# Kernel optimization log

Measured on AMD Instinct MI355X. Metric: run time of the kernel, lower is better.

The kernel has to match this reference:

```python
import jax, jax.numpy as jnp
import numpy as np

N_EMBD = 768
N_HEAD = 12
B, T = 4, 2048
EPS = 1e-5


def layernorm(x, w, b):
    mu = jnp.mean(x, axis=-1, keepdims=True)
    var = jnp.mean(jnp.square(x - mu), axis=-1, keepdims=True)
    return (x - mu) * jax.lax.rsqrt(var + EPS) * w + b


def setup_inputs() -> dict:
    key = jax.random.key(0)
    ks = jax.random.split(key, 6)
    C = N_EMBD
    s = 0.02
    return {
        "x": jax.random.normal(ks[0], (B, T, C), jnp.float32),
        "ln1_w": jnp.ones((C,), jnp.float32),
        "ln1_b": jnp.zeros((C,), jnp.float32),
        "W_qkv": jax.random.normal(ks[1], (C, 3 * C), jnp.float32) * s,
        "b_qkv": jnp.zeros((3 * C,), jnp.float32),
        "W_attnproj": jax.random.normal(ks[2], (C, C), jnp.float32) * s,
        "b_attnproj": jnp.zeros((C,), jnp.float32),
        "ln2_w": jnp.ones((C,), jnp.float32),
        "ln2_b": jnp.zeros((C,), jnp.float32),
        "W_fc": jax.random.normal(ks[3], (C, 4 * C), jnp.float32) * s,
        "b_fc": jnp.zeros((4 * C,), jnp.float32),
        "W_mlpproj": jax.random.normal(ks[4], (4 * C, C), jnp.float32) * s,
        "b_mlpproj": jnp.zeros((C,), jnp.float32),
    }


def reference(x, ln1_w, ln1_b, W_qkv, b_qkv, W_attnproj, b_attnproj,
              ln2_w, ln2_b, W_fc, b_fc, W_mlpproj, b_mlpproj):
    Bx, Tx, C = x.shape
    H = N_HEAD
    Dh = C // H

    # --- attention branch ---
    h = layernorm(x, ln1_w, ln1_b)
    qkv = h @ W_qkv + b_qkv                       # [B, T, 3C]
    q, k, v = jnp.split(qkv, 3, axis=-1)
    q = q.reshape(Bx, Tx, H, Dh).transpose(0, 2, 1, 3)  # [B, H, T, Dh]
    k = k.reshape(Bx, Tx, H, Dh).transpose(0, 2, 1, 3)
    v = v.reshape(Bx, Tx, H, Dh).transpose(0, 2, 1, 3)
    att = jnp.einsum('bhqd,bhkd->bhqk', q, k) * (1.0 / np.sqrt(Dh))
    att = jax.nn.softmax(att, axis=-1)            # full softmax attention (no mask)
    y = jnp.einsum('bhqk,bhkd->bhqd', att, v)     # [B, H, T, Dh]
    y = y.transpose(0, 2, 1, 3).reshape(Bx, Tx, C)
    y = y @ W_attnproj + b_attnproj
    x = x + y

    # --- MLP branch ---
    h = layernorm(x, ln2_w, ln2_b)
    h = jax.nn.gelu(h @ W_fc + b_fc, approximate=False)
    h = h @ W_mlpproj + b_mlpproj
    return x + h
```

## Files before the change

### kernel.cpp

```cpp
#include <hip/hip_runtime.h>

typedef __bf16 bf16x8 __attribute__((ext_vector_type(8)));
typedef __bf16 bf16x4 __attribute__((ext_vector_type(4)));
typedef float f32x4 __attribute__((ext_vector_type(4)));
typedef unsigned short u16;
typedef unsigned long long u64;

#define GL2LDS(gp, lp) __builtin_amdgcn_global_load_lds(                      \
    (const __attribute__((address_space(1))) void*)(gp),                      \
    (__attribute__((address_space(3))) void*)(lp), 16, 0, 0)

__device__ __forceinline__ u16 f2u(float f) {
    __bf16 h = (__bf16)f;
    return __builtin_bit_cast(u16, h);
}

__device__ __forceinline__ float fexp2(float x) {
    float r;
    asm("v_exp_f32 %0, %1" : "=v"(r) : "v"(x));
    return r;
}

__device__ __forceinline__ float frcp(float x) {
    float r;
    asm("v_rcp_f32 %0, %1" : "=v"(r) : "v"(x));
    return r;
}

__device__ __forceinline__ float gelu(float x) {
    const float a = x * x;
    const float b = fmaf(a, 0.10294323f, 2.30220795f);
    const float u = fexp2(x * b);
    const float r = frcp(1.0f + u);
    return (x > 8.0f) ? x : x * u * r;
}

template <int N>
__device__ __forceinline__ void waitv() {
    if constexpr (N == 0) asm volatile("s_waitcnt vmcnt(0)" ::: "memory");
    else if constexpr (N == 4) asm volatile("s_waitcnt vmcnt(4)" ::: "memory");
    else if constexpr (N == 5) asm volatile("s_waitcnt vmcnt(5)" ::: "memory");
    else if constexpr (N == 6) asm volatile("s_waitcnt vmcnt(6)" ::: "memory");
}

__device__ __forceinline__ f32x4 mfma16(bf16x8 a, bf16x8 b, f32x4 c) {
    return __builtin_amdgcn_mfma_f32_16x16x32_bf16(a, b, c, 0, 0, 0);
}

struct TransDesc {
    const float* W[4];
    u16* Wt[4];
    int K[4], N[4], end[4];
};

__global__ __launch_bounds__(256) void transpose4_kernel(TransDesc d) {
    __shared__ float tile[32][33];
    const int b = blockIdx.x;
    const int i = (b >= d.end[0]) + (b >= d.end[1]) + (b >= d.end[2]);
    const float* __restrict__ W = d.W[i];
    u16* __restrict__ Wt = d.Wt[i];
    const int K = d.K[i], N = d.N[i];
    const int local = b - (i == 0 ? 0 : d.end[i - 1]);
    const int gx = N >> 5;
    const int n0 = (local % gx) * 32, k0 = (local / gx) * 32;
    const int tx = threadIdx.x & 31, ty = threadIdx.x >> 5;
#pragma unroll
    for (int r = 0; r < 4; r++)
        tile[ty + 8 * r][tx] = W[(size_t)(k0 + ty + 8 * r) * N + n0 + tx];
    __syncthreads();
#pragma unroll
    for (int r = 0; r < 4; r++)
        Wt[(size_t)(n0 + ty + 8 * r) * K + k0 + tx] = f2u(tile[tx][ty + 8 * r]);
}

__global__ __launch_bounds__(256) void ln_kernel(
    const float* __restrict__ xin, const float* __restrict__ wgt,
    const float* __restrict__ bia, u16* __restrict__ outp) {
    const int row = blockIdx.x, t = threadIdx.x;
    const float* xr = xin + (size_t)row * 768;
    float v0 = xr[t], v1 = xr[t + 256], v2 = xr[t + 512];
    float s = v0 + v1 + v2;
    float ss = v0 * v0 + v1 * v1 + v2 * v2;
#pragma unroll
    for (int off = 32; off; off >>= 1) {
        s += __shfl_xor(s, off);
        ss += __shfl_xor(ss, off);
    }
    __shared__ float red[8];
    const int w = t >> 6;
    if ((t & 63) == 0) { red[w] = s; red[4 + w] = ss; }
    __syncthreads();
    s  = red[0] + red[1] + red[2] + red[3];
    ss = red[4] + red[5] + red[6] + red[7];
    const float mu = s * (1.f / 768.f);
    const float var = ss * (1.f / 768.f) - mu * mu;
    const float rs = rsqrtf(var + 1e-5f);
    u16* orow = outp + (size_t)row * 768;
    orow[t]       = f2u((v0 - mu) * rs * wgt[t]       + bia[t]);
    orow[t + 256] = f2u((v1 - mu) * rs * wgt[t + 256] + bia[t + 256]);
    orow[t + 512] = f2u((v2 - mu) * rs * wgt[t + 512] + bia[t + 512]);
}

template <int EPI>
__global__ __launch_bounds__(256, 3) void gemm96(
    const u16* __restrict__ A, const u16* __restrict__ Bt,
    const float* __restrict__ bias, void* __restrict__ outp,
    u16* __restrict__ vt, int M, int N, int K) {
    __shared__ __align__(16) u16 As[2][4096];
    __shared__ __align__(16) u16 Bs[2][6144];
    const int t = threadIdx.x;
    const int lane = t & 63, w = t >> 6;
    const int wg0 = blockIdx.y * gridDim.x + blockIdx.x;
    const int xcd = wg0 & 7, loc = wg0 >> 3;
    const int gx = gridDim.x, gy = gridDim.y;
    const int m0 = (xcd * (gy >> 3) + loc / gx) * 128;
    const int n0 = (loc % gx) * 192;
    const int wm = (w >> 1) * 64, wn = (w & 1) * 96;
    const int lq = lane & 15, g = lane >> 4;

    f32x4 acc[4][6];
#pragma unroll
    for (int i = 0; i < 4; i++)
#pragma unroll
        for (int j = 0; j < 6; j++) acc[i][j] = (f32x4){0.f, 0.f, 0.f, 0.f};

    const int srow = t >> 2;
    const int scol = ((t & 3) ^ ((t >> 3) & 3)) * 8;
    const u16* gA0 = A + (size_t)(m0 + srow) * K + scol;
    const u16* gA1 = A + (size_t)(m0 + 64 + srow) * K + scol;
    const u16* gB0 = Bt + (size_t)(n0 + srow) * K + scol;
    const u16* gB1 = Bt + (size_t)(n0 + 64 + srow) * K + scol;
    const u16* gB2 = Bt + (size_t)(n0 + 128 + srow) * K + scol;

    const int cph = (g ^ ((lq >> 1) & 3)) << 4;
    const int KT = K >> 5;

#define STAGE96(buf, kt)                                                      \
    do {                                                                      \
        const int ko_ = (kt) << 5;                                            \
        GL2LDS(gA0 + ko_, (char*)As[buf] + w * 1024);                         \
        GL2LDS(gA1 + ko_, (char*)As[buf] + 4096 + w * 1024);                  \
        GL2LDS(gB0 + ko_, (char*)Bs[buf] + w * 1024);                         \
        GL2LDS(gB1 + ko_, (char*)Bs[buf] + 4096 + w * 1024);                  \
        GL2LDS(gB2 + ko_, (char*)Bs[buf] + 8192 + w * 1024);                  \
    } while (0)

    STAGE96(0, 0);
    STAGE96(1, 1);
    for (int kt = 0; kt < KT; ++kt) {
        if (kt + 1 < KT) waitv<5>(); else waitv<0>();
        __builtin_amdgcn_s_barrier();
        __builtin_amdgcn_sched_barrier(0);
        const char* rA = (char*)As[kt & 1] + (wm + lq) * 64 + cph;
        const char* rB = (char*)Bs[kt & 1] + (wn + lq) * 64 + cph;
        bf16x8 af[4];
#pragma unroll
        for (int m = 0; m < 4; m++) af[m] = *(const bf16x8*)(rA + m * 1024);
        __builtin_amdgcn_s_setprio(1);
#pragma unroll
        for (int n = 0; n < 6; n++) {
            const bf16x8 bfr = *(const bf16x8*)(rB + n * 1024);
#pragma unroll
            for (int m = 0; m < 4; m++)
                acc[m][n] = mfma16(af[m], bfr, acc[m][n]);
        }
        __builtin_amdgcn_s_setprio(0);
        __builtin_amdgcn_sched_barrier(0);
        __builtin_amdgcn_s_barrier();
        if (kt + 2 < KT) STAGE96(kt & 1, kt + 2);
    }
#undef STAGE96

#pragma unroll
    for (int n = 0; n < 6; n++) {
        const int col = n0 + wn + 16 * n + lq;
        const float bv = bias[col];
#pragma unroll
        for (int m = 0; m < 4; m++) {
            const int rbase = m0 + wm + 16 * m + 4 * g;
            if constexpr (EPI == 0) {
                if (col < 1536) {
                    const float qs = (col < 768) ? 0.18033688f : 1.0f;
#pragma unroll
                    for (int r = 0; r < 4; r++) {
                        const size_t idx = (size_t)(rbase + r) * N + col;
                        ((u16*)outp)[idx] = f2u((acc[m][n][r] + bv) * qs);
                    }
                } else {
                    const int d = col - 1536;
                    bf16x4 pk;
#pragma unroll
                    for (int r = 0; r < 4; r++)
                        pk[r] = (__bf16)(acc[m][n][r] + bv);
                    u16* vrow = vt +
                        ((size_t)((rbase >> 11) * 12 + (d >> 6)) * 64 + (d & 63)) * 2048 +
                        (rbase & 2047);
                    *(u64*)vrow = __builtin_bit_cast(u64, pk);
                }
            } else {
#pragma unroll
                for (int r = 0; r < 4; r++) {
                    const size_t idx = (size_t)(rbase + r) * N + col;
                    ((u16*)outp)[idx] = f2u(gelu(acc[m][n][r] + bv));
                }
            }
        }
    }
}

__global__ __launch_bounds__(256, 3) void gemm_k64(
    const u16* __restrict__ A, const u16* __restrict__ Bt,
    const float* __restrict__ bias, const float* __restrict__ res,
    float* __restrict__ outp, int M, int N, int K) {
    __shared__ __align__(16) u16 As[2][4096];
    __shared__ __align__(16) u16 Bs[2][8192];
    const int t = threadIdx.x;
    const int lane = t & 63, w = t >> 6;
    const int wg0 = blockIdx.y * gridDim.x + blockIdx.x;
    const int xcd = wg0 & 7, loc = wg0 >> 3;
    const int gx = gridDim.x, gy = gridDim.y;
    const int m0 = (xcd * (gy >> 3) + loc / gx) * 64;
    const int n0 = (loc % gx) * 128;
    const int wm = (w >> 1) * 32, wn = (w & 1) * 64;
    const int lq = lane & 15, g = lane >> 4;

    f32x4 acc[2][4];
#pragma unroll
    for (int i = 0; i < 2; i++)
#pragma unroll
        for (int j = 0; j < 4; j++) acc[i][j] = (f32x4){0.f, 0.f, 0.f, 0.f};

    const int srow8 = w * 8 + (lane >> 3);
    const int scol = ((lane & 7) ^ (lane >> 3)) * 8;
    const u16* gA_0 = A + (size_t)(m0 + srow8) * K + scol;
    const u16* gA_1 = A + (size_t)(m0 + 32 + srow8) * K + scol;
    const u16* gB_0 = Bt + (size_t)(n0 + srow8) * K + scol;
    const u16* gB_1 = Bt + (size_t)(n0 + 32 + srow8) * K + scol;
    const u16* gB_2 = Bt + (size_t)(n0 + 64 + srow8) * K + scol;
    const u16* gB_3 = Bt + (size_t)(n0 + 96 + srow8) * K + scol;

    const int KT = K >> 6;

#define STAGE64(buf, kt)                                                      \
    do {                                                                      \
        const int ko_ = (kt) << 6;                                            \
        GL2LDS(gA_0 + ko_, (char*)As[buf] + w * 1024);                        \
        GL2LDS(gA_1 + ko_, (char*)As[buf] + 4096 + w * 1024);                 \
        GL2LDS(gB_0 + ko_, (char*)Bs[buf] + w * 1024);                        \
        GL2LDS(gB_1 + ko_, (char*)Bs[buf] + 4096 + w * 1024);                 \
        GL2LDS(gB_2 + ko_, (char*)Bs[buf] + 8192 + w * 1024);                 \
        GL2LDS(gB_3 + ko_, (char*)Bs[buf] + 12288 + w * 1024);                \
    } while (0)

    STAGE64(0, 0);
    STAGE64(1, 1);
    for (int kt = 0; kt < KT; ++kt) {
        if (kt + 1 < KT) waitv<6>(); else waitv<0>();
        __builtin_amdgcn_s_barrier();
        __builtin_amdgcn_sched_barrier(0);
        const char* aB = (char*)As[kt & 1] + (wm + lq) * 128;
        const char* bB = (char*)Bs[kt & 1] + (wn + lq) * 128;
        const int sw = lq & 7;
#pragma unroll
        for (int s = 0; s < 2; s++) {
            const int co = (((s << 2) + g) ^ sw) << 4;
            bf16x8 af[2], bfr[4];
#pragma unroll
            for (int m = 0; m < 2; m++)
                af[m] = *(const bf16x8*)(aB + m * 2048 + co);
#pragma unroll
            for (int n = 0; n < 4; n++)
                bfr[n] = *(const bf16x8*)(bB + n * 2048 + co);
            __builtin_amdgcn_s_setprio(1);
#pragma unroll
            for (int m = 0; m < 2; m++)
#pragma unroll
                for (int n = 0; n < 4; n++)
                    acc[m][n] = mfma16(af[m], bfr[n], acc[m][n]);
            __builtin_amdgcn_s_setprio(0);
        }
        __builtin_amdgcn_sched_barrier(0);
        __builtin_amdgcn_s_barrier();
        if (kt + 2 < KT) STAGE64(kt & 1, kt + 2);
    }
#undef STAGE64

#pragma unroll
    for (int n = 0; n < 4; n++) {
        const int col = n0 + wn + 16 * n + lq;
        const float bv = bias[col];
#pragma unroll
        for (int m = 0; m < 2; m++) {
            const int rbase = m0 + wm + 16 * m + 4 * g;
#pragma unroll
            for (int r = 0; r < 4; r++) {
                const size_t idx = (size_t)(rbase + r) * N + col;
                outp[idx] = acc[m][n][r] + bv + res[idx];
            }
        }
    }
}

__global__ __launch_bounds__(256, 3) void attn_kernel(
    const u16* __restrict__ qkv, const u16* __restrict__ Vt,
    u16* __restrict__ y) {
    __shared__ __align__(16) u16 Ks[2][4096];
    __shared__ __align__(16) u16 Vts[2][4096];
    __shared__ __align__(16) u16 Ps[4][2048];
    const int t = threadIdx.x, lane = t & 63, w = t >> 6;
    int wg = blockIdx.y * gridDim.x + blockIdx.x;
    wg = (wg & 7) * ((gridDim.x * gridDim.y) >> 3) + (wg >> 3);
    const int bh = wg / gridDim.x;
    const int b = bh / 12, h = bh % 12;
    const int q0 = (wg % gridDim.x) * 128 + w * 32;
    const int lq = lane & 15, g = lane >> 4;
    const int swz = (lq & 7) << 4;

    bf16x8 qf[2][2];
#pragma unroll
    for (int qh = 0; qh < 2; qh++) {
        const u16* qp =
            qkv + (size_t)(b * 2048 + q0 + qh * 16 + lq) * 2304 + h * 64 + g * 8;
        qf[qh][0] = *(const bf16x8*)(qp);
        qf[qh][1] = *(const bf16x8*)(qp + 32);
    }
    bf16x8 ones;
#pragma unroll
    for (int i = 0; i < 8; i++) ones[i] = (__bf16)1.0f;

    f32x4 acc_o[2][4], acc_s[2];
#pragma unroll
    for (int qh = 0; qh < 2; qh++) {
        acc_s[qh] = (f32x4){0.f, 0.f, 0.f, 0.f};
#pragma unroll
        for (int f = 0; f < 4; f++) acc_o[qh][f] = (f32x4){0.f, 0.f, 0.f, 0.f};
    }

    const int srow = t >> 3, sc = (t & 7) ^ (srow & 7);
    const u16* kg = qkv + 768 + h * 64 + sc * 8 + (size_t)(b * 2048 + srow) * 2304;
    const u16* vg = Vt + (size_t)(bh * 64 + srow) * 2048 + sc * 8;

#define STAGEKV(buf, kt)                                                      \
    do {                                                                      \
        const int kn_ = (kt) * 64;                                            \
        GL2LDS(kg + (size_t)kn_ * 2304, (char*)Ks[buf] + w * 1024);           \
        GL2LDS(kg + (size_t)(kn_ + 32) * 2304,                                \
               (char*)Ks[buf] + w * 1024 + 4096);                             \
        GL2LDS(vg + kn_, (char*)Vts[buf] + w * 1024);                         \
        GL2LDS(vg + 32 * 2048 + kn_, (char*)Vts[buf] + w * 1024 + 4096);      \
    } while (0)

    STAGEKV(0, 0);
    STAGEKV(1, 1);
    for (int kt = 0; kt < 32; ++kt) {
        const int buf = kt & 1;
        if (kt + 1 < 32) waitv<4>(); else waitv<0>();
        __builtin_amdgcn_s_barrier();
        __builtin_amdgcn_sched_barrier(0);
        const char* KB = (const char*)Ks[buf];
        const char* VB = (const char*)Vts[buf];

        f32x4 st[2][4];
        __builtin_amdgcn_s_setprio(1);
#pragma unroll
        for (int kb = 0; kb < 4; kb++) {
            st[0][kb] = (f32x4){0.f, 0.f, 0.f, 0.f};
            st[1][kb] = (f32x4){0.f, 0.f, 0.f, 0.f};
            const char* kr = KB + (kb * 16 + lq) * 128;
#pragma unroll
            for (int dh = 0; dh < 2; dh++) {
                const bf16x8 kf =
                    *(const bf16x8*)(kr + ((((dh << 2) + g) << 4) ^ swz));
                st[0][kb] = mfma16(kf, qf[0][dh], st[0][kb]);
                st[1][kb] = mfma16(kf, qf[1][dh], st[1][kb]);
            }
        }
        __builtin_amdgcn_s_setprio(0);

#pragma unroll
        for (int qh = 0; qh < 2; qh++) {
            char* pw = (char*)Ps[w] + (qh * 16 + lq) * 128 + ((g & 1) << 3);
#pragma unroll
            for (int kb = 0; kb < 4; kb++) {
                bf16x4 pb;
#pragma unroll
                for (int r = 0; r < 4; r++)
                    pb[r] = (__bf16)fexp2(st[qh][kb][r]);
                *(u64*)(pw + ((((kb << 1) + (g >> 1)) << 4) ^ swz)) =
                    __builtin_bit_cast(u64, pb);
            }
        }

        __builtin_amdgcn_s_setprio(1);
#pragma unroll
        for (int kk = 0; kk < 2; kk++) {
            const int co = ((kk << 2) + g) << 4;
            bf16x8 vf[4];
#pragma unroll
            for (int f = 0; f < 4; f++)
                vf[f] = *(const bf16x8*)(VB + (16 * f + lq) * 128 + (co ^ swz));
#pragma unroll
            for (int qh = 0; qh < 2; qh++) {
                const bf16x8 pf = *(const bf16x8*)(
                    (const char*)Ps[w] + (qh * 16 + lq) * 128 + (co ^ swz));
#pragma unroll
                for (int f = 0; f < 4; f++)
                    acc_o[qh][f] = mfma16(vf[f], pf, acc_o[qh][f]);
                acc_s[qh] = mfma16(ones, pf, acc_s[qh]);
            }
        }
        __builtin_amdgcn_s_setprio(0);
        __builtin_amdgcn_sched_barrier(0);
        __builtin_amdgcn_s_barrier();
        if (kt + 2 < 32) STAGEKV(buf, kt + 2);
    }
#undef STAGEKV

#pragma unroll
    for (int qh = 0; qh < 2; qh++) {
        const float rinv = frcp(acc_s[qh][0]);
        char* yb = (char*)(y + (size_t)(b * 2048 + q0 + qh * 16 + lq) * 768 +
                           h * 64);
#pragma unroll
        for (int f = 0; f < 4; f++) {
            bf16x4 pk;
#pragma unroll
            for (int r = 0; r < 4; r++) pk[r] = (__bf16)(acc_o[qh][f][r] * rinv);
            *(u64*)(yb + f * 32 + g * 8) = __builtin_bit_cast(u64, pk);
        }
    }
}

extern "C" void kernel_launch(void* const* d_in, const int* in_sizes, int n_in,
                              void* d_out, int out_size, void* d_ws,
                              size_t ws_size, hipStream_t stream) {
    const float* x    = (const float*)d_in[0];
    const float* ln1w = (const float*)d_in[1];
    const float* ln1b = (const float*)d_in[2];
    const float* Wqkv = (const float*)d_in[3];
    const float* bqkv = (const float*)d_in[4];
    const float* Wap  = (const float*)d_in[5];
    const float* bap  = (const float*)d_in[6];
    const float* ln2w = (const float*)d_in[7];
    const float* ln2b = (const float*)d_in[8];
    const float* Wfc  = (const float*)d_in[9];
    const float* bfc  = (const float*)d_in[10];
    const float* Wmp  = (const float*)d_in[11];
    const float* bmp  = (const float*)d_in[12];
    float* out = (float*)d_out;

    char* ws = (char*)d_ws;
    u16* Wt_qkv = (u16*)(ws);
    u16* Wt_ap  = (u16*)(ws + 3538944);
    u16* Wt_fc  = (u16*)(ws + 4718592);
    u16* Wt_mp  = (u16*)(ws + 9437184);
    u16* bufA   = (u16*)(ws + 14155776);
    u16* bufB   = (u16*)(ws + 26738688);
    u16* VtBuf  = (u16*)(ws + 64487424);

    TransDesc td;
    td.W[0] = Wqkv; td.Wt[0] = Wt_qkv; td.K[0] = 768;  td.N[0] = 2304; td.end[0] = 1728;
    td.W[1] = Wap;  td.Wt[1] = Wt_ap;  td.K[1] = 768;  td.N[1] = 768;  td.end[1] = 2304;
    td.W[2] = Wfc;  td.Wt[2] = Wt_fc;  td.K[2] = 768;  td.N[2] = 3072; td.end[2] = 4608;
    td.W[3] = Wmp;  td.Wt[3] = Wt_mp;  td.K[3] = 3072; td.N[3] = 768;  td.end[3] = 6912;
    transpose4_kernel<<<6912, 256, 0, stream>>>(td);

    ln_kernel<<<8192, 256, 0, stream>>>(x, ln1w, ln1b, bufA);
    gemm96<0><<<dim3(12, 64), 256, 0, stream>>>(
        bufA, Wt_qkv, bqkv, bufB, VtBuf, 8192, 2304, 768);
    attn_kernel<<<dim3(16, 48), 256, 0, stream>>>(bufB, VtBuf, bufA);
    gemm_k64<<<dim3(6, 128), 256, 0, stream>>>(
        bufA, Wt_ap, bap, x, out, 8192, 768, 768);
    ln_kernel<<<8192, 256, 0, stream>>>(out, ln2w, ln2b, bufA);
    gemm96<2><<<dim3(16, 64), 256, 0, stream>>>(
        bufA, Wt_fc, bfc, bufB, nullptr, 8192, 3072, 768);
    gemm_k64<<<dim3(6, 128), 256, 0, stream>>>(
        bufB, Wt_mp, bmp, out, out, 8192, 768, 3072);
}
```

Baseline: 256.0 us.

## Merge weight transpose with first layernorm; single-buffer attention KV for higher occupancy

Folds the weight-transpose kernel and the first layernorm into one launch whose block index picks the job, saving one launch and letting the two independent workloads overlap. Attention K/V staging goes from double-buffered to single-buffered with a full vmcnt(0) wait each iteration. This cuts LDS use, so launch bounds can ask for 4 blocks per CU instead of 3. The trade is that global loads are no longer prefetched behind compute in each block, and the code relies on the extra resident blocks to hide that latency.

```diff
diff --git a/kernel.cpp b/kernel.cpp
--- a/kernel.cpp
+++ b/kernel.cpp
@@ -38,7 +38,6 @@
 template <int N>
 __device__ __forceinline__ void waitv() {
     if constexpr (N == 0) asm volatile("s_waitcnt vmcnt(0)" ::: "memory");
-    else if constexpr (N == 4) asm volatile("s_waitcnt vmcnt(4)" ::: "memory");
     else if constexpr (N == 5) asm volatile("s_waitcnt vmcnt(5)" ::: "memory");
     else if constexpr (N == 6) asm volatile("s_waitcnt vmcnt(6)" ::: "memory");
 }
@@ -47,30 +46,61 @@
     return __builtin_amdgcn_mfma_f32_16x16x32_bf16(a, b, c, 0, 0, 0);
 }
 
-struct TransDesc {
+struct PreDesc {
     const float* W[4];
     u16* Wt[4];
     int K[4], N[4], end[4];
+    const float* x;
+    const float* lw;
+    const float* lb;
+    u16* lo;
 };
 
-__global__ __launch_bounds__(256) void transpose4_kernel(TransDesc d) {
-    __shared__ float tile[32][33];
-    const int b = blockIdx.x;
-    const int i = (b >= d.end[0]) + (b >= d.end[1]) + (b >= d.end[2]);
-    const float* __restrict__ W = d.W[i];
-    u16* __restrict__ Wt = d.Wt[i];
-    const int K = d.K[i], N = d.N[i];
-    const int local = b - (i == 0 ? 0 : d.end[i - 1]);
-    const int gx = N >> 5;
-    const int n0 = (local % gx) * 32, k0 = (local / gx) * 32;
-    const int tx = threadIdx.x & 31, ty = threadIdx.x >> 5;
-#pragma unroll
-    for (int r = 0; r < 4; r++)
-        tile[ty + 8 * r][tx] = W[(size_t)(k0 + ty + 8 * r) * N + n0 + tx];
-    __syncthreads();
-#pragma unroll
-    for (int r = 0; r < 4; r++)
-        Wt[(size_t)(n0 + ty + 8 * r) * K + k0 + tx] = f2u(tile[tx][ty + 8 * r]);
+__global__ __launch_bounds__(256) void pre_kernel(PreDesc d) {
+    const int blk = blockIdx.x;
+    if (blk < d.end[3]) {
+        __shared__ float tile[32][33];
+        const int i = (blk >= d.end[0]) + (blk >= d.end[1]) + (blk >= d.end[2]);
+        const float* __restrict__ W = d.W[i];
+        u16* __restrict__ Wt = d.Wt[i];
+        const int K = d.K[i], N = d.N[i];
+        const int local = blk - (i == 0 ? 0 : d.end[i - 1]);
+        const int gx = N >> 5;
+        const int n0 = (local % gx) * 32, k0 = (local / gx) * 32;
+        const int tx = threadIdx.x & 31, ty = threadIdx.x >> 5;
+#pragma unroll
+        for (int r = 0; r < 4; r++)
+            tile[ty + 8 * r][tx] = W[(size_t)(k0 + ty + 8 * r) * N + n0 + tx];
+        __syncthreads();
+#pragma unroll
+        for (int r = 0; r < 4; r++)
+            Wt[(size_t)(n0 + ty + 8 * r) * K + k0 + tx] =
+                f2u(tile[tx][ty + 8 * r]);
+    } else {
+        const int row = blk - d.end[3], t = threadIdx.x;
+        const float* xr = d.x + (size_t)row * 768;
+        float v0 = xr[t], v1 = xr[t + 256], v2 = xr[t + 512];
+        float s = v0 + v1 + v2;
+        float ss = v0 * v0 + v1 * v1 + v2 * v2;
+#pragma unroll
+        for (int off = 32; off; off >>= 1) {
+            s += __shfl_xor(s, off);
+            ss += __shfl_xor(ss, off);
+        }
+        __shared__ float red[8];
+        const int w = t >> 6;
+        if ((t & 63) == 0) { red[w] = s; red[4 + w] = ss; }
+        __syncthreads();
+        s  = red[0] + red[1] + red[2] + red[3];
+        ss = red[4] + red[5] + red[6] + red[7];
+        const float mu = s * (1.f / 768.f);
+        const float var = ss * (1.f / 768.f) - mu * mu;
+        const float rs = rsqrtf(var + 1e-5f);
+        u16* orow = d.lo + (size_t)row * 768;
+        orow[t]       = f2u((v0 - mu) * rs * d.lw[t]       + d.lb[t]);
+        orow[t + 256] = f2u((v1 - mu) * rs * d.lw[t + 256] + d.lb[t + 256]);
+        orow[t + 512] = f2u((v2 - mu) * rs * d.lw[t + 512] + d.lb[t + 512]);
+    }
 }
 
 __global__ __launch_bounds__(256) void ln_kernel(
@@ -301,11 +331,11 @@
     }
 }
 
-__global__ __launch_bounds__(256, 3) void attn_kernel(
+__global__ __launch_bounds__(256, 4) void attn_kernel(
     const u16* __restrict__ qkv, const u16* __restrict__ Vt,
     u16* __restrict__ y) {
-    __shared__ __align__(16) u16 Ks[2][4096];
-    __shared__ __align__(16) u16 Vts[2][4096];
+    __shared__ __align__(16) u16 Ks[4096];
+    __shared__ __align__(16) u16 Vts[4096];
     __shared__ __align__(16) u16 Ps[4][2048];
     const int t = threadIdx.x, lane = t & 63, w = t >> 6;
     int wg = blockIdx.y * gridDim.x + blockIdx.x;
@@ -340,25 +370,17 @@
     const u16* kg = qkv + 768 + h * 64 + sc * 8 + (size_t)(b * 2048 + srow) * 2304;
     const u16* vg = Vt + (size_t)(bh * 64 + srow) * 2048 + sc * 8;
 
-#define STAGEKV(buf, kt)                                                      \
-    do {                                                                      \
-        const int kn_ = (kt) * 64;                                            \
-        GL2LDS(kg + (size_t)kn_ * 2304, (char*)Ks[buf] + w * 1024);           \
-        GL2LDS(kg + (size_t)(kn_ + 32) * 2304,                                \
-               (char*)Ks[buf] + w * 1024 + 4096);                             \
-        GL2LDS(vg + kn_, (char*)Vts[buf] + w * 1024);                         \
-        GL2LDS(vg + 32 * 2048 + kn_, (char*)Vts[buf] + w * 1024 + 4096);      \
-    } while (0)
-
-    STAGEKV(0, 0);
-    STAGEKV(1, 1);
     for (int kt = 0; kt < 32; ++kt) {
-        const int buf = kt & 1;
-        if (kt + 1 < 32) waitv<4>(); else waitv<0>();
-        __builtin_amdgcn_s_barrier();
-        __builtin_amdgcn_sched_barrier(0);
-        const char* KB = (const char*)Ks[buf];
-        const char* VB = (const char*)Vts[buf];
+        const int kn = kt * 64;
+        GL2LDS(kg + (size_t)kn * 2304, (char*)Ks + w * 1024);
+        GL2LDS(kg + (size_t)(kn + 32) * 2304, (char*)Ks + w * 1024 + 4096);
+        GL2LDS(vg + kn, (char*)Vts + w * 1024);
+        GL2LDS(vg + 32 * 2048 + kn, (char*)Vts + w * 1024 + 4096);
+        waitv<0>();
+        __builtin_amdgcn_s_barrier();
+        __builtin_amdgcn_sched_barrier(0);
+        const char* KB = (const char*)Ks;
+        const char* VB = (const char*)Vts;
 
         f32x4 st[2][4];
         __builtin_amdgcn_s_setprio(1);
@@ -412,9 +434,7 @@
         __builtin_amdgcn_s_setprio(0);
         __builtin_amdgcn_sched_barrier(0);
         __builtin_amdgcn_s_barrier();
-        if (kt + 2 < 32) STAGEKV(buf, kt + 2);
-    }
-#undef STAGEKV
+    }
 
 #pragma unroll
     for (int qh = 0; qh < 2; qh++) {
@@ -458,14 +478,14 @@
     u16* bufB   = (u16*)(ws + 26738688);
     u16* VtBuf  = (u16*)(ws + 64487424);
 
-    TransDesc td;
-    td.W[0] = Wqkv; td.Wt[0] = Wt_qkv; td.K[0] = 768;  td.N[0] = 2304; td.end[0] = 1728;
-    td.W[1] = Wap;  td.Wt[1] = Wt_ap;  td.K[1] = 768;  td.N[1] = 768;  td.end[1] = 2304;
-    td.W[2] = Wfc;  td.Wt[2] = Wt_fc;  td.K[2] = 768;  td.N[2] = 3072; td.end[2] = 4608;
-    td.W[3] = Wmp;  td.Wt[3] = Wt_mp;  td.K[3] = 3072; td.N[3] = 768;  td.end[3] = 6912;
-    transpose4_kernel<<<6912, 256, 0, stream>>>(td);
-
-    ln_kernel<<<8192, 256, 0, stream>>>(x, ln1w, ln1b, bufA);
+    PreDesc pd;
+    pd.W[0] = Wqkv; pd.Wt[0] = Wt_qkv; pd.K[0] = 768;  pd.N[0] = 2304; pd.end[0] = 1728;
+    pd.W[1] = Wap;  pd.Wt[1] = Wt_ap;  pd.K[1] = 768;  pd.N[1] = 768;  pd.end[1] = 2304;
+    pd.W[2] = Wfc;  pd.Wt[2] = Wt_fc;  pd.K[2] = 768;  pd.N[2] = 3072; pd.end[2] = 4608;
+    pd.W[3] = Wmp;  pd.Wt[3] = Wt_mp;  pd.K[3] = 3072; pd.N[3] = 768;  pd.end[3] = 6912;
+    pd.x = x; pd.lw = ln1w; pd.lb = ln1b; pd.lo = bufA;
+    pre_kernel<<<15104, 256, 0, stream>>>(pd);
+
     gemm96<0><<<dim3(12, 64), 256, 0, stream>>>(
         bufA, Wt_qkv, bqkv, bufB, VtBuf, 8192, 2304, 768);
     attn_kernel<<<dim3(16, 48), 256, 0, stream>>>(bufB, VtBuf, bufA);
```

Result: no change. 253.4 us (median of 2 runs) (-1.0%).
